# Kernel optimization log

Hardware: AMD Instinct MI355X
Metric: run time of the kernel (lower is better)

The kernel has to match this reference:

```python
import jax, jax.numpy as jnp
import numpy as np

H = 1024
V = 50257
B = 64
T = 512


def setup_inputs() -> dict:
    key = jax.random.key(0)
    ks = jax.random.split(key, 16)
    s = 0.02
    return {
        "input_seq": jax.random.randint(ks[0], (B,), 0, V, dtype=jnp.int32),
        "last_hidden": jax.random.normal(ks[1], (1, B, H), dtype=jnp.float32),
        "encoder_outputs": jax.random.normal(ks[2], (B, T, H), dtype=jnp.float32),
        "emb": jax.random.normal(ks[3], (V, H), dtype=jnp.float32) * s,
        "W_ih": jax.random.normal(ks[4], (3 * H, H), dtype=jnp.float32) * s,
        "W_hh": jax.random.normal(ks[5], (3 * H, H), dtype=jnp.float32) * s,
        "b_ih": jnp.zeros((3 * H,), jnp.float32),
        "b_hh": jnp.zeros((3 * H,), jnp.float32),
        "W_a": jax.random.normal(ks[6], (H, H), dtype=jnp.float32) * s,
        "b_a": jnp.zeros((H,), jnp.float32),
        "W_c": jax.random.normal(ks[7], (H, 2 * H), dtype=jnp.float32) * s,
        "b_c": jnp.zeros((H,), jnp.float32),
        "W_o": jax.random.normal(ks[8], (V, H), dtype=jnp.float32) * s,
        "b_o": jnp.zeros((V,), jnp.float32),
    }


def reference(input_seq, last_hidden, encoder_outputs, emb, W_ih, W_hh, b_ih, b_hh,
              W_a, b_a, W_c, b_c, W_o, b_o):
    # Embedding lookup (dropout is identity in eval)
    x = emb[input_seq]                      # [B, H]
    h0 = last_hidden[0]                     # [B, H] (num_layers == 1)

    # Single GRU step, torch gate order (r, z, n)
    gi = x @ W_ih.T + b_ih                  # [B, 3H]
    gh = h0 @ W_hh.T + b_hh                 # [B, 3H]
    r = jax.nn.sigmoid(gi[:, :H] + gh[:, :H])
    z = jax.nn.sigmoid(gi[:, H:2 * H] + gh[:, H:2 * H])
    n = jnp.tanh(gi[:, 2 * H:] + r * gh[:, 2 * H:])
    h = (1.0 - z) * n + z * h0              # [B, H]

    # Attention, method='general': batched (replaces per-batch torch.mm loop)
    energy = jnp.einsum('bth,oh->bto', encoder_outputs, W_a) + b_a  # [B, T, H]
    scores = jnp.einsum('bh,bth->bt', h, energy)                    # [B, T]
    attn_w = jax.nn.softmax(scores, axis=1)                         # [B, T]
    context = jnp.einsum('bt,bth->bh', attn_w, encoder_outputs)     # [B, H]

    concat_input = jnp.concatenate([h, context], axis=1)            # [B, 2H]
    concat_output = jnp.tanh(concat_input @ W_c.T + b_c)            # [B, H]
    output = concat_output @ W_o.T + b_o                            # [B, V]
    hidden = h[None]                                                # [1, B, H]
    return (output, hidden)
```

## Files before the change

kernel.cpp:

```cpp
#include <hip/hip_runtime.h>
#include <hip/hip_bf16.h>
#include <cstdint>
#include <cstddef>

#define H 1024
#define V 50257
#define B 64
#define T 512

typedef __attribute__((ext_vector_type(8))) short bf16x8;
typedef __attribute__((ext_vector_type(4))) float f32x4;

__device__ __forceinline__ float sigmoidf_(float x) { return 1.0f / (1.0f + expf(-x)); }

__device__ __forceinline__ unsigned short f2bf_rn(float x) {
    __hip_bfloat16 h = __float2bfloat16(x);
    return __builtin_bit_cast(unsigned short, h);
}

__device__ __forceinline__ void gl_lds16(const float* g, float* l) {
    __builtin_amdgcn_global_load_lds(
        (const __attribute__((address_space(1))) unsigned*)g,
        (__attribute__((address_space(3))) unsigned*)l, 16, 0, 0);
}

__device__ __forceinline__ void wave_vm_drain() {
    asm volatile("s_waitcnt vmcnt(0)" ::: "memory");
    __builtin_amdgcn_sched_barrier(0);
}

__global__ void k_prep(const int* __restrict__ seq, const float* __restrict__ emb,
                       const float* __restrict__ h0,
                       unsigned short* __restrict__ X_bf,
                       unsigned short* __restrict__ h0_bf) {
    int i = blockIdx.x * 256 + threadIdx.x;
    int b = i >> 10, h = i & 1023;
    X_bf[i] = f2bf_rn(emb[(size_t)seq[b] * H + h]);
    h0_bf[i] = f2bf_rn(h0[i]);
}

__global__ __launch_bounds__(256) void k_mfma_bt(
    const unsigned short* __restrict__ A0, const unsigned short* __restrict__ A1, int lda,
    const float* __restrict__ B0, const float* __restrict__ B1, int ldb,
    float* __restrict__ C0, float* __restrict__ C1, int N, int KC) {
    __shared__ __align__(16) float Bs[2][128 * 64];
    const unsigned short* A = blockIdx.z ? A1 : A0;
    const float* Bm = blockIdx.z ? B1 : B0;
    float* C = (blockIdx.z ? C1 : C0) + (size_t)blockIdx.y * 64 * N;
    const int t = threadIdx.x;
    const int w = t >> 6, lane = t & 63;
    const int li = lane & 15, qu = lane >> 4;
    const int n0 = blockIdx.x * 128;
    const int k0 = blockIdx.y * KC;
    const int nsteps = KC >> 6;

    f32x4 acc[4][2];
#pragma unroll
    for (int ms = 0; ms < 4; ++ms)
#pragma unroll
        for (int nt = 0; nt < 2; ++nt) acc[ms][nt] = (f32x4){0.f, 0.f, 0.f, 0.f};

#define STG(BUF, KK)                                                            \
    {                                                                           \
        _Pragma("unroll")                                                       \
        for (int j = 0; j < 8; ++j) {                                           \
            int cidx = (w * 8 + j) * 64 + lane;                                 \
            int row = cidx >> 4, cs = cidx & 15;                                \
            int cg = cs ^ (row & 15);                                           \
            const float* gp = Bm + (size_t)(n0 + row) * ldb + (KK) + cg * 4;    \
            gl_lds16(gp, &Bs[BUF][(w * 8 + j) * 256]);                          \
        }                                                                       \
    }

    STG(0, k0)

    for (int kt = 0; kt < nsteps; ++kt) {
        const int buf = kt & 1;
        wave_vm_drain();
        if (kt + 1 < nsteps) STG(buf ^ 1, k0 + (kt + 1) * 64)

        const int kk = k0 + kt * 64;
#pragma unroll
        for (int ks = 0; ks < 2; ++ks) {
            bf16x8 af[4];
#pragma unroll
            for (int ms = 0; ms < 4; ++ms)
                af[ms] = *(const bf16x8*)&A[(size_t)(ms * 16 + li) * lda + kk + ks * 32 + qu * 8];
#pragma unroll
            for (int nt = 0; nt < 2; ++nt) {
                int row = w * 32 + nt * 16 + li;
                int cc0 = ks * 8 + qu * 2;
                float4 x0 = *(const float4*)&Bs[buf][row * 64 + ((cc0)     ^ (row & 15)) * 4];
                float4 x1 = *(const float4*)&Bs[buf][row * 64 + ((cc0 + 1) ^ (row & 15)) * 4];
                bf16x8 bfr;
                bfr[0] = (short)f2bf_rn(x0.x); bfr[1] = (short)f2bf_rn(x0.y);
                bfr[2] = (short)f2bf_rn(x0.z); bfr[3] = (short)f2bf_rn(x0.w);
                bfr[4] = (short)f2bf_rn(x1.x); bfr[5] = (short)f2bf_rn(x1.y);
                bfr[6] = (short)f2bf_rn(x1.z); bfr[7] = (short)f2bf_rn(x1.w);
#pragma unroll
                for (int ms = 0; ms < 4; ++ms)
                    acc[ms][nt] = __builtin_amdgcn_mfma_f32_16x16x32_bf16(
                        af[ms], bfr, acc[ms][nt], 0, 0, 0);
            }
        }
    }
#undef STG

#pragma unroll
    for (int nt = 0; nt < 2; ++nt) {
        int col = n0 + w * 32 + nt * 16 + li;
#pragma unroll
        for (int ms = 0; ms < 4; ++ms)
#pragma unroll
            for (int j = 0; j < 4; ++j)
                C[(size_t)(ms * 16 + qu * 4 + j) * N + col] = acc[ms][nt][j];
    }
}

__global__ __launch_bounds__(256) void k_mfma_wa(const unsigned short* __restrict__ cat_bf,
                                                 const float* __restrict__ Wa,
                                                 float* __restrict__ Pu) {
    const int t = threadIdx.x;
    const int w = t >> 6, lane = t & 63;
    const int li = lane & 15, qu = lane >> 4;
    const int n0 = blockIdx.x * 128;
    const int k0 = blockIdx.y * 256;

    f32x4 acc[4][2];
#pragma unroll
    for (int ms = 0; ms < 4; ++ms)
#pragma unroll
        for (int nt = 0; nt < 2; ++nt) acc[ms][nt] = (f32x4){0.f, 0.f, 0.f, 0.f};

    for (int kt = 0; kt < 4; ++kt) {
        const int kk = k0 + kt * 64;
#pragma unroll
        for (int ks = 0; ks < 2; ++ks) {
            bf16x8 af[4];
#pragma unroll
            for (int ms = 0; ms < 4; ++ms)
                af[ms] = *(const bf16x8*)&cat_bf[(size_t)(ms * 16 + li) * 2048 + kk + ks * 32 + qu * 8];
            const int kb = kk + ks * 32 + qu * 8;
#pragma unroll
            for (int nt = 0; nt < 2; ++nt) {
                int col = n0 + w * 32 + nt * 16 + li;
                bf16x8 bfr;
#pragma unroll
                for (int e = 0; e < 8; ++e)
                    bfr[e] = (short)f2bf_rn(Wa[(size_t)(kb + e) * H + col]);
#pragma unroll
                for (int ms = 0; ms < 4; ++ms)
                    acc[ms][nt] = __builtin_amdgcn_mfma_f32_16x16x32_bf16(
                        af[ms], bfr, acc[ms][nt], 0, 0, 0);
            }
        }
    }
    float* C = Pu + (size_t)blockIdx.y * 64 * H;
#pragma unroll
    for (int nt = 0; nt < 2; ++nt) {
        int col = n0 + w * 32 + nt * 16 + li;
#pragma unroll
        for (int ms = 0; ms < 4; ++ms)
#pragma unroll
            for (int j = 0; j < 4; ++j)
                C[(size_t)(ms * 16 + qu * 4 + j) * H + col] = acc[ms][nt][j];
    }
}

__global__ void k_gru(const float* __restrict__ Pgi, const float* __restrict__ Pgh,
                      const float* __restrict__ bih, const float* __restrict__ bhh,
                      const float* __restrict__ h0, unsigned short* __restrict__ cat_bf,
                      float* __restrict__ hid) {
    int i = blockIdx.x * 256 + threadIdx.x;
    int b = i >> 10, h = i & 1023;
    float gr = bih[h], gz = bih[H + h], gn = bih[2 * H + h];
    float hr = bhh[h], hz = bhh[H + h], hn = bhh[2 * H + h];
#pragma unroll
    for (int kt = 0; kt < 4; ++kt) {
        const float* pi = Pgi + (size_t)kt * B * 3 * H + (size_t)b * 3 * H;
        const float* ph = Pgh + (size_t)kt * B * 3 * H + (size_t)b * 3 * H;
        gr += pi[h]; gz += pi[H + h]; gn += pi[2 * H + h];
        hr += ph[h]; hz += ph[H + h]; hn += ph[2 * H + h];
    }
    float r = sigmoidf_(gr + hr);
    float z = sigmoidf_(gz + hz);
    float n = tanhf(gn + r * hn);
    float hv = (1.0f - z) * n + z * h0[i];
    cat_bf[(size_t)b * 2048 + h] = f2bf_rn(hv);
    hid[i] = hv;
}

__global__ __launch_bounds__(256) void k_flash(const float* __restrict__ Pu,
                                               const float* __restrict__ enc,
                                               float* __restrict__ Pm,
                                               float* __restrict__ Pl,
                                               float* __restrict__ Pc) {
    const int b = blockIdx.x >> 4, ch = blockIdx.x & 15;
    const int w = threadIdx.x >> 6, lane = threadIdx.x & 63;

    float4 uu[4];
#pragma unroll
    for (int it = 0; it < 4; ++it) {
        int col = (it * 64 + lane) * 4;
        float4 s = *(const float4*)&Pu[(size_t)b * H + col];
#pragma unroll
        for (int kt = 1; kt < 4; ++kt) {
            float4 p = *(const float4*)&Pu[(size_t)kt * B * H + (size_t)b * H + col];
            s.x += p.x; s.y += p.y; s.z += p.z; s.w += p.w;
        }
        uu[it] = s;
    }

    float m = -3.4e38f, l = 0.f;
    float4 c[4] = {{0,0,0,0},{0,0,0,0},{0,0,0,0},{0,0,0,0}};
    const float* ebase = enc + ((size_t)b * T + ch * 32 + w * 8) * H;

#pragma unroll 2
    for (int tt = 0; tt < 8; ++tt) {
        float4 e[4];
#pragma unroll
        for (int it = 0; it < 4; ++it)
            e[it] = *(const float4*)&ebase[(size_t)tt * H + (it * 64 + lane) * 4];
        float s = 0.f;
#pragma unroll
        for (int it = 0; it < 4; ++it)
            s += uu[it].x * e[it].x + uu[it].y * e[it].y +
                 uu[it].z * e[it].z + uu[it].w * e[it].w;
#pragma unroll
        for (int o = 32; o; o >>= 1) s += __shfl_xor(s, o, 64);
        float mn = fmaxf(m, s);
        float scale = __expf(m - mn);
        float p = __expf(s - mn);
        l = l * scale + p;
#pragma unroll
        for (int it = 0; it < 4; ++it) {
            c[it].x = fmaf(p, e[it].x, c[it].x * scale);
            c[it].y = fmaf(p, e[it].y, c[it].y * scale);
            c[it].z = fmaf(p, e[it].z, c[it].z * scale);
            c[it].w = fmaf(p, e[it].w, c[it].w * scale);
        }
        m = mn;
    }

    __shared__ float Lm[4], Ll[4];
    __shared__ __align__(16) float Lc[4][H];
#pragma unroll
    for (int it = 0; it < 4; ++it)
        *(float4*)&Lc[w][(it * 64 + lane) * 4] = c[it];
    if (lane == 0) { Lm[w] = m; Ll[w] = l; }
    __syncthreads();

    float M = fmaxf(fmaxf(Lm[0], Lm[1]), fmaxf(Lm[2], Lm[3]));
    float e0 = __expf(Lm[0] - M), e1 = __expf(Lm[1] - M),
          e2 = __expf(Lm[2] - M), e3 = __expf(Lm[3] - M);
    float L = Ll[0] * e0 + Ll[1] * e1 + Ll[2] * e2 + Ll[3] * e3;
    int col = threadIdx.x * 4;
    float4 c0 = *(const float4*)&Lc[0][col];
    float4 c1 = *(const float4*)&Lc[1][col];
    float4 c2 = *(const float4*)&Lc[2][col];
    float4 c3 = *(const float4*)&Lc[3][col];
    float4 cc;
    cc.x = c0.x * e0 + c1.x * e1 + c2.x * e2 + c3.x * e3;
    cc.y = c0.y * e0 + c1.y * e1 + c2.y * e2 + c3.y * e3;
    cc.z = c0.z * e0 + c1.z * e1 + c2.z * e2 + c3.z * e3;
    cc.w = c0.w * e0 + c1.w * e1 + c2.w * e2 + c3.w * e3;
    const int rec = blockIdx.x;
    if (threadIdx.x == 0) { Pm[rec] = M; Pl[rec] = L; }
    *(float4*)&Pc[(size_t)rec * H + col] = cc;
}

__global__ void k_fcomb(const float* __restrict__ Pm, const float* __restrict__ Pl,
                        const float* __restrict__ Pc, unsigned short* __restrict__ cat_bf) {
    const int b = blockIdx.x;
    const int col = threadIdx.x * 4;
    float M = -3.4e38f;
#pragma unroll
    for (int i = 0; i < 16; ++i) M = fmaxf(M, Pm[b * 16 + i]);
    float L = 0.f;
    float4 cc = {0, 0, 0, 0};
#pragma unroll 4
    for (int i = 0; i < 16; ++i) {
        float wgt = __expf(Pm[b * 16 + i] - M);
        L += Pl[b * 16 + i] * wgt;
        float4 p = *(const float4*)&Pc[(size_t)(b * 16 + i) * H + col];
        cc.x += wgt * p.x; cc.y += wgt * p.y;
        cc.z += wgt * p.z; cc.w += wgt * p.w;
    }
    float inv = 1.0f / L;
    ushort4 o;
    o.x = f2bf_rn(cc.x * inv); o.y = f2bf_rn(cc.y * inv);
    o.z = f2bf_rn(cc.z * inv); o.w = f2bf_rn(cc.w * inv);
    *(ushort4*)&cat_bf[(size_t)b * 2048 + 1024 + col] = o;
}

__global__ void k_co(const float* __restrict__ Pc, const float* __restrict__ bc,
                     unsigned short* __restrict__ co_bf) {
    int i = blockIdx.x * 256 + threadIdx.x;
    int h = i & 1023;
    float s = bc[h];
#pragma unroll
    for (int kt = 0; kt < 4; ++kt) s += Pc[kt * (B * H) + i];
    co_bf[i] = f2bf_rn(tanhf(s));
}

__global__ __launch_bounds__(256) void k_out_mfma(const unsigned short* __restrict__ co_bf,
                                                  const float* __restrict__ Wo,
                                                  const float* __restrict__ bo,
                                                  float* __restrict__ out) {
    __shared__ __align__(16) float Bs[2][128 * 64];
    const int t = threadIdx.x;
    const int w = t >> 6, lane = t & 63;
    const int li = lane & 15, qu = lane >> 4;
    const int v0 = blockIdx.x * 128;

    f32x4 acc[4][2];
#pragma unroll
    for (int ms = 0; ms < 4; ++ms)
#pragma unroll
        for (int nt = 0; nt < 2; ++nt) acc[ms][nt] = (f32x4){0.f, 0.f, 0.f, 0.f};

#define STAGE(BUF, KK)                                                          \
    {                                                                           \
        _Pragma("unroll")                                                       \
        for (int j = 0; j < 8; ++j) {                                           \
            int cidx = (w * 8 + j) * 64 + lane;                                 \
            int row = cidx >> 4, cs = cidx & 15;                                \
            int cg = cs ^ (row & 15);                                           \
            int vr = v0 + row; if (vr >= V) vr = V - 1;                         \
            const float* gp = Wo + (size_t)vr * H + (KK) + cg * 4;              \
            gl_lds16(gp, &Bs[BUF][(w * 8 + j) * 256]);                          \
        }                                                                       \
    }

    STAGE(0, 0)

    for (int kt = 0; kt < 16; ++kt) {
        const int buf = kt & 1;
        wave_vm_drain();
        if (kt < 15) STAGE(buf ^ 1, (kt + 1) * 64)

        const int kk = kt * 64;
#pragma unroll
        for (int ks = 0; ks < 2; ++ks) {
            bf16x8 af[4];
#pragma unroll
            for (int ms = 0; ms < 4; ++ms)
                af[ms] = *(const bf16x8*)&co_bf[(size_t)(ms * 16 + li) * H + kk + ks * 32 + qu * 8];
#pragma unroll
            for (int nt = 0; nt < 2; ++nt) {
                int row = w * 32 + nt * 16 + li;
                int cc0 = ks * 8 + qu * 2;
                float4 x0 = *(const float4*)&Bs[buf][row * 64 + ((cc0)     ^ (row & 15)) * 4];
                float4 x1 = *(const float4*)&Bs[buf][row * 64 + ((cc0 + 1) ^ (row & 15)) * 4];
                bf16x8 bfr;
                bfr[0] = (short)f2bf_rn(x0.x); bfr[1] = (short)f2bf_rn(x0.y);
                bfr[2] = (short)f2bf_rn(x0.z); bfr[3] = (short)f2bf_rn(x0.w);
                bfr[4] = (short)f2bf_rn(x1.x); bfr[5] = (short)f2bf_rn(x1.y);
                bfr[6] = (short)f2bf_rn(x1.z); bfr[7] = (short)f2bf_rn(x1.w);
#pragma unroll
                for (int ms = 0; ms < 4; ++ms)
                    acc[ms][nt] = __builtin_amdgcn_mfma_f32_16x16x32_bf16(
                        af[ms], bfr, acc[ms][nt], 0, 0, 0);
            }
        }
    }
#undef STAGE

#pragma unroll
    for (int nt = 0; nt < 2; ++nt) {
        int v = v0 + w * 32 + nt * 16 + li;
        if (v < V) {
            float bov = bo[v];
#pragma unroll
            for (int ms = 0; ms < 4; ++ms)
#pragma unroll
                for (int j = 0; j < 4; ++j)
                    out[(size_t)(ms * 16 + qu * 4 + j) * V + v] = acc[ms][nt][j] + bov;
        }
    }
}

extern "C" void kernel_launch(void* const* d_in, const int* in_sizes, int n_in,
                              void* d_out, int out_size, void* d_ws, size_t ws_size,
                              hipStream_t stream) {
    (void)in_sizes; (void)n_in; (void)out_size; (void)ws_size;
    const int*   seq = (const int*)d_in[0];
    const float* h0  = (const float*)d_in[1];
    const float* enc = (const float*)d_in[2];
    const float* emb = (const float*)d_in[3];
    const float* Wih = (const float*)d_in[4];
    const float* Whh = (const float*)d_in[5];
    const float* bih = (const float*)d_in[6];
    const float* bhh = (const float*)d_in[7];
    const float* Wa  = (const float*)d_in[8];
    const float* Wc  = (const float*)d_in[10];
    const float* bc  = (const float*)d_in[11];
    const float* Wo  = (const float*)d_in[12];
    const float* bo  = (const float*)d_in[13];

    float* out = (float*)d_out;
    float* hid = out + (size_t)B * V;

    float* ws   = (float*)d_ws;
    float* Pgi  = ws;
    float* Pgh  = Pgi + 786432;
    float* Pu   = Pgh + 786432;
    float* Pm   = Pu + 262144;
    float* Pl   = Pm + 1024;
    float* Pc   = Pl + 1024;
    float* Pcg  = Pc + 1048576;
    unsigned short* X_bf  = (unsigned short*)(Pcg + 262144);
    unsigned short* h0_bf = X_bf + 65536;
    unsigned short* cat_bf = h0_bf + 65536;
    unsigned short* co_bf  = cat_bf + 131072;

    k_prep<<<256, 256, 0, stream>>>(seq, emb, h0, X_bf, h0_bf);
    k_mfma_bt<<<dim3(24, 4, 2), 256, 0, stream>>>(X_bf, h0_bf, H, Wih, Whh, H,
                                                  Pgi, Pgh, 3 * H, 256);
    k_gru<<<256, 256, 0, stream>>>(Pgi, Pgh, bih, bhh, h0, cat_bf, hid);
    k_mfma_wa<<<dim3(8, 4), 256, 0, stream>>>(cat_bf, Wa, Pu);
    k_flash<<<1024, 256, 0, stream>>>(Pu, enc, Pm, Pl, Pc);
    k_fcomb<<<64, 256, 0, stream>>>(Pm, Pl, Pc, cat_bf);
    k_mfma_bt<<<dim3(8, 4, 1), 256, 0, stream>>>(cat_bf, cat_bf, 2 * H, Wc, Wc, 2 * H,
                                                 Pcg, Pcg, H, 512);
    k_co<<<256, 256, 0, stream>>>(Pcg, bc, co_bf);
    k_out_mfma<<<(V + 127) / 128, 256, 0, stream>>>(co_bf, Wo, bo, out);
}
```

Before: 142.4 us.

## Deepen GEMM prefetch pipeline and fuse embedding prep into gates GEMM

```diff
diff --git a/kernel.cpp b/kernel.cpp
--- a/kernel.cpp
+++ b/kernel.cpp
@@ -24,29 +24,125 @@
         (__attribute__((address_space(3))) unsigned*)l, 16, 0, 0);
 }
 
-__device__ __forceinline__ void wave_vm_drain() {
+__device__ __forceinline__ void wait_vm8() {
+    asm volatile("s_waitcnt vmcnt(8)" ::: "memory");
+    __builtin_amdgcn_sched_barrier(0);
+}
+__device__ __forceinline__ void wait_vm0() {
     asm volatile("s_waitcnt vmcnt(0)" ::: "memory");
     __builtin_amdgcn_sched_barrier(0);
 }
-
-__global__ void k_prep(const int* __restrict__ seq, const float* __restrict__ emb,
-                       const float* __restrict__ h0,
-                       unsigned short* __restrict__ X_bf,
-                       unsigned short* __restrict__ h0_bf) {
-    int i = blockIdx.x * 256 + threadIdx.x;
-    int b = i >> 10, h = i & 1023;
-    X_bf[i] = f2bf_rn(emb[(size_t)seq[b] * H + h]);
-    h0_bf[i] = f2bf_rn(h0[i]);
-}
-
-__global__ __launch_bounds__(256) void k_mfma_bt(
-    const unsigned short* __restrict__ A0, const unsigned short* __restrict__ A1, int lda,
-    const float* __restrict__ B0, const float* __restrict__ B1, int ldb,
-    float* __restrict__ C0, float* __restrict__ C1, int N, int KC) {
+__device__ __forceinline__ void lds_war_guard() {
+    asm volatile("s_waitcnt lgkmcnt(0)" ::: "memory");
+    __builtin_amdgcn_sched_barrier(0);
+}
+
+__global__ __launch_bounds__(256) void k_gates(const int* __restrict__ seq,
+                                               const float* __restrict__ emb,
+                                               const float* __restrict__ h0,
+                                               const float* __restrict__ Wih,
+                                               const float* __restrict__ Whh,
+                                               float* __restrict__ Pgi,
+                                               float* __restrict__ Pgh) {
     __shared__ __align__(16) float Bs[2][128 * 64];
-    const unsigned short* A = blockIdx.z ? A1 : A0;
-    const float* Bm = blockIdx.z ? B1 : B0;
-    float* C = (blockIdx.z ? C1 : C0) + (size_t)blockIdx.y * 64 * N;
+    const int z = blockIdx.z;
+    const float* Bm = z ? Whh : Wih;
+    float* C = (z ? Pgh : Pgi) + (size_t)blockIdx.y * 64 * (3 * H);
+    const int t = threadIdx.x;
+    const int w = t >> 6, lane = t & 63;
+    const int li = lane & 15, qu = lane >> 4;
+    const int n0 = blockIdx.x * 128;
+    const int k0 = blockIdx.y * 256;
+    const int N = 3 * H;
+
+    const float* Arow[4];
+#pragma unroll
+    for (int ms = 0; ms < 4; ++ms) {
+        int m = ms * 16 + li;
+        Arow[ms] = z ? (h0 + (size_t)m * H) : (emb + (size_t)seq[m] * H);
+    }
+
+    f32x4 acc[4][2];
+#pragma unroll
+    for (int ms = 0; ms < 4; ++ms)
+#pragma unroll
+        for (int nt = 0; nt < 2; ++nt) acc[ms][nt] = (f32x4){0.f, 0.f, 0.f, 0.f};
+
+#define STG(BUF, KK)                                                            \
+    {                                                                           \
+        _Pragma("unroll")                                                       \
+        for (int j = 0; j < 8; ++j) {                                           \
+            int cidx = (w * 8 + j) * 64 + lane;                                 \
+            int row = cidx >> 4, cs = cidx & 15;                                \
+            int cg = cs ^ (row & 15);                                           \
+            const float* gp = Bm + (size_t)(n0 + row) * H + (KK) + cg * 4;      \
+            gl_lds16(gp, &Bs[BUF][(w * 8 + j) * 256]);                          \
+        }                                                                       \
+    }
+
+#define CONSUME(BUF, KK)                                                        \
+    {                                                                           \
+        _Pragma("unroll")                                                       \
+        for (int ks = 0; ks < 2; ++ks) {                                        \
+            bf16x8 af[4];                                                       \
+            _Pragma("unroll")                                                   \
+            for (int ms = 0; ms < 4; ++ms) {                                    \
+                float4 a0 = *(const float4*)&Arow[ms][(KK) + ks * 32 + qu * 8]; \
+                float4 a1 = *(const float4*)&Arow[ms][(KK) + ks * 32 + qu * 8 + 4]; \
+                af[ms][0] = (short)f2bf_rn(a0.x); af[ms][1] = (short)f2bf_rn(a0.y); \
+                af[ms][2] = (short)f2bf_rn(a0.z); af[ms][3] = (short)f2bf_rn(a0.w); \
+                af[ms][4] = (short)f2bf_rn(a1.x); af[ms][5] = (short)f2bf_rn(a1.y); \
+                af[ms][6] = (short)f2bf_rn(a1.z); af[ms][7] = (short)f2bf_rn(a1.w); \
+            }                                                                   \
+            _Pragma("unroll")                                                   \
+            for (int nt = 0; nt < 2; ++nt) {                                    \
+                int row = w * 32 + nt * 16 + li;                                \
+                int cc0 = ks * 8 + qu * 2;                                      \
+                float4 x0 = *(const float4*)&Bs[BUF][row * 64 + ((cc0)     ^ (row & 15)) * 4]; \
+                float4 x1 = *(const float4*)&Bs[BUF][row * 64 + ((cc0 + 1) ^ (row & 15)) * 4]; \
+                bf16x8 bfr;                                                     \
+                bfr[0] = (short)f2bf_rn(x0.x); bfr[1] = (short)f2bf_rn(x0.y);   \
+                bfr[2] = (short)f2bf_rn(x0.z); bfr[3] = (short)f2bf_rn(x0.w);   \
+                bfr[4] = (short)f2bf_rn(x1.x); bfr[5] = (short)f2bf_rn(x1.y);   \
+                bfr[6] = (short)f2bf_rn(x1.z); bfr[7] = (short)f2bf_rn(x1.w);   \
+                _Pragma("unroll")                                               \
+                for (int ms = 0; ms < 4; ++ms)                                  \
+                    acc[ms][nt] = __builtin_amdgcn_mfma_f32_16x16x32_bf16(      \
+                        af[ms], bfr, acc[ms][nt], 0, 0, 0);                     \
+            }                                                                   \
+        }                                                                       \
+    }
+
+    STG(0, k0)
+    STG(1, k0 + 64)
+    for (int kt = 0; kt < 3; ++kt) {
+        const int buf = kt & 1;
+        wait_vm8();
+        CONSUME(buf, k0 + kt * 64)
+        if (kt + 2 < 4) { lds_war_guard(); STG(buf, k0 + (kt + 2) * 64) }
+    }
+    wait_vm0();
+    CONSUME(1, k0 + 3 * 64)
+#undef STG
+#undef CONSUME
+
+#pragma unroll
+    for (int nt = 0; nt < 2; ++nt) {
+        int col = n0 + w * 32 + nt * 16 + li;
+#pragma unroll
+        for (int ms = 0; ms < 4; ++ms)
+#pragma unroll
+            for (int j = 0; j < 4; ++j)
+                C[(size_t)(ms * 16 + qu * 4 + j) * N + col] = acc[ms][nt][j];
+    }
+}
+
+__global__ __launch_bounds__(256) void k_mfma_bt(const unsigned short* __restrict__ A,
+                                                 int lda,
+                                                 const float* __restrict__ Bm, int ldb,
+                                                 float* __restrict__ Cp, int N, int KC) {
+    __shared__ __align__(16) float Bs[2][128 * 64];
+    float* C = Cp + (size_t)blockIdx.y * 64 * N;
     const int t = threadIdx.x;
     const int w = t >> 6, lane = t & 63;
     const int li = lane & 15, qu = lane >> 4;
@@ -72,39 +168,45 @@
         }                                                                       \
     }
 
+#define CONSUME(BUF, KK)                                                        \
+    {                                                                           \
+        _Pragma("unroll")                                                       \
+        for (int ks = 0; ks < 2; ++ks) {                                        \
+            bf16x8 af[4];                                                       \
+            _Pragma("unroll")                                                   \
+            for (int ms = 0; ms < 4; ++ms)                                      \
+                af[ms] = *(const bf16x8*)&A[(size_t)(ms * 16 + li) * lda + (KK) + ks * 32 + qu * 8]; \
+            _Pragma("unroll")                                                   \
+            for (int nt = 0; nt < 2; ++nt) {                                    \
+                int row = w * 32 + nt * 16 + li;                                \
+                int cc0 = ks * 8 + qu * 2;                                      \
+                float4 x0 = *(const float4*)&Bs[BUF][row * 64 + ((cc0)     ^ (row & 15)) * 4]; \
+                float4 x1 = *(const float4*)&Bs[BUF][row * 64 + ((cc0 + 1) ^ (row & 15)) * 4]; \
+                bf16x8 bfr;                                                     \
+                bfr[0] = (short)f2bf_rn(x0.x); bfr[1] = (short)f2bf_rn(x0.y);   \
+                bfr[2] = (short)f2bf_rn(x0.z); bfr[3] = (short)f2bf_rn(x0.w);   \
+                bfr[4] = (short)f2bf_rn(x1.x); bfr[5] = (short)f2bf_rn(x1.y);   \
+                bfr[6] = (short)f2bf_rn(x1.z); bfr[7] = (short)f2bf_rn(x1.w);   \
+                _Pragma("unroll")                                               \
+                for (int ms = 0; ms < 4; ++ms)                                  \
+                    acc[ms][nt] = __builtin_amdgcn_mfma_f32_16x16x32_bf16(      \
+                        af[ms], bfr, acc[ms][nt], 0, 0, 0);                     \
+            }                                                                   \
+        }                                                                       \
+    }
+
     STG(0, k0)
-
-    for (int kt = 0; kt < nsteps; ++kt) {
+    STG(1, k0 + 64)
+    for (int kt = 0; kt < nsteps - 1; ++kt) {
         const int buf = kt & 1;
-        wave_vm_drain();
-        if (kt + 1 < nsteps) STG(buf ^ 1, k0 + (kt + 1) * 64)
-
-        const int kk = k0 + kt * 64;
-#pragma unroll
-        for (int ks = 0; ks < 2; ++ks) {
-            bf16x8 af[4];
-#pragma unroll
-            for (int ms = 0; ms < 4; ++ms)
-                af[ms] = *(const bf16x8*)&A[(size_t)(ms * 16 + li) * lda + kk + ks * 32 + qu * 8];
-#pragma unroll
-            for (int nt = 0; nt < 2; ++nt) {
-                int row = w * 32 + nt * 16 + li;
-                int cc0 = ks * 8 + qu * 2;
-                float4 x0 = *(const float4*)&Bs[buf][row * 64 + ((cc0)     ^ (row & 15)) * 4];
-                float4 x1 = *(const float4*)&Bs[buf][row * 64 + ((cc0 + 1) ^ (row & 15)) * 4];
-                bf16x8 bfr;
-                bfr[0] = (short)f2bf_rn(x0.x); bfr[1] = (short)f2bf_rn(x0.y);
-                bfr[2] = (short)f2bf_rn(x0.z); bfr[3] = (short)f2bf_rn(x0.w);
-                bfr[4] = (short)f2bf_rn(x1.x); bfr[5] = (short)f2bf_rn(x1.y);
-                bfr[6] = (short)f2bf_rn(x1.z); bfr[7] = (short)f2bf_rn(x1.w);
-#pragma unroll
-                for (int ms = 0; ms < 4; ++ms)
-                    acc[ms][nt] = __builtin_amdgcn_mfma_f32_16x16x32_bf16(
-                        af[ms], bfr, acc[ms][nt], 0, 0, 0);
-            }
-        }
-    }
+        wait_vm8();
+        CONSUME(buf, k0 + kt * 64)
+        if (kt + 2 < nsteps) { lds_war_guard(); STG(buf, k0 + (kt + 2) * 64) }
+    }
+    wait_vm0();
+    CONSUME((nsteps - 1) & 1, k0 + (nsteps - 1) * 64)
 #undef STG
+#undef CONSUME
 
 #pragma unroll
     for (int nt = 0; nt < 2; ++nt) {
@@ -332,39 +434,45 @@
         }                                                                       \
     }
 
+#define CONSUME(BUF, KK)                                                        \
+    {                                                                           \
+        _Pragma("unroll")                                                       \
+        for (int ks = 0; ks < 2; ++ks) {                                        \
+            bf16x8 af[4];                                                       \
+            _Pragma("unroll")                                                   \
+            for (int ms = 0; ms < 4; ++ms)                                      \
+                af[ms] = *(const bf16x8*)&co_bf[(size_t)(ms * 16 + li) * H + (KK) + ks * 32 + qu * 8]; \
+            _Pragma("unroll")                                                   \
+            for (int nt = 0; nt < 2; ++nt) {                                    \
+                int row = w * 32 + nt * 16 + li;                                \
+                int cc0 = ks * 8 + qu * 2;                                      \
+                float4 x0 = *(const float4*)&Bs[BUF][row * 64 + ((cc0)     ^ (row & 15)) * 4]; \
+                float4 x1 = *(const float4*)&Bs[BUF][row * 64 + ((cc0 + 1) ^ (row & 15)) * 4]; \
+                bf16x8 bfr;                                                     \
+                bfr[0] = (short)f2bf_rn(x0.x); bfr[1] = (short)f2bf_rn(x0.y);   \
+                bfr[2] = (short)f2bf_rn(x0.z); bfr[3] = (short)f2bf_rn(x0.w);   \
+                bfr[4] = (short)f2bf_rn(x1.x); bfr[5] = (short)f2bf_rn(x1.y);   \
+                bfr[6] = (short)f2bf_rn(x1.z); bfr[7] = (short)f2bf_rn(x1.w);   \
+                _Pragma("unroll")                                               \
+                for (int ms = 0; ms < 4; ++ms)                                  \
+                    acc[ms][nt] = __builtin_amdgcn_mfma_f32_16x16x32_bf16(      \
+                        af[ms], bfr, acc[ms][nt], 0, 0, 0);                     \
+            }                                                                   \
+        }                                                                       \
+    }
+
     STAGE(0, 0)
-
-    for (int kt = 0; kt < 16; ++kt) {
+    STAGE(1, 64)
+    for (int kt = 0; kt < 15; ++kt) {
         const int buf = kt & 1;
-        wave_vm_drain();
-        if (kt < 15) STAGE(buf ^ 1, (kt + 1) * 64)
-
-        const int kk = kt * 64;
-#pragma unroll
-        for (int ks = 0; ks < 2; ++ks) {
-            bf16x8 af[4];
-#pragma unroll
-            for (int ms = 0; ms < 4; ++ms)
-                af[ms] = *(const bf16x8*)&co_bf[(size_t)(ms * 16 + li) * H + kk + ks * 32 + qu * 8];
-#pragma unroll
-            for (int nt = 0; nt < 2; ++nt) {
-                int row = w * 32 + nt * 16 + li;
-                int cc0 = ks * 8 + qu * 2;
-                float4 x0 = *(const float4*)&Bs[buf][row * 64 + ((cc0)     ^ (row & 15)) * 4];
-                float4 x1 = *(const float4*)&Bs[buf][row * 64 + ((cc0 + 1) ^ (row & 15)) * 4];
-                bf16x8 bfr;
-                bfr[0] = (short)f2bf_rn(x0.x); bfr[1] = (short)f2bf_rn(x0.y);
-                bfr[2] = (short)f2bf_rn(x0.z); bfr[3] = (short)f2bf_rn(x0.w);
-                bfr[4] = (short)f2bf_rn(x1.x); bfr[5] = (short)f2bf_rn(x1.y);
-                bfr[6] = (short)f2bf_rn(x1.z); bfr[7] = (short)f2bf_rn(x1.w);
-#pragma unroll
-                for (int ms = 0; ms < 4; ++ms)
-                    acc[ms][nt] = __builtin_amdgcn_mfma_f32_16x16x32_bf16(
-                        af[ms], bfr, acc[ms][nt], 0, 0, 0);
-            }
-        }
-    }
+        wait_vm8();
+        CONSUME(buf, kt * 64)
+        if (kt + 2 < 16) { lds_war_guard(); STAGE(buf, (kt + 2) * 64) }
+    }
+    wait_vm0();
+    CONSUME(1, 15 * 64)
 #undef STAGE
+#undef CONSUME
 
 #pragma unroll
     for (int nt = 0; nt < 2; ++nt) {
@@ -409,20 +517,15 @@
     float* Pl   = Pm + 1024;
     float* Pc   = Pl + 1024;
     float* Pcg  = Pc + 1048576;
-    unsigned short* X_bf  = (unsigned short*)(Pcg + 262144);
-    unsigned short* h0_bf = X_bf + 65536;
-    unsigned short* cat_bf = h0_bf + 65536;
+    unsigned short* cat_bf = (unsigned short*)(Pcg + 262144);
     unsigned short* co_bf  = cat_bf + 131072;
 
-    k_prep<<<256, 256, 0, stream>>>(seq, emb, h0, X_bf, h0_bf);
-    k_mfma_bt<<<dim3(24, 4, 2), 256, 0, stream>>>(X_bf, h0_bf, H, Wih, Whh, H,
-                                                  Pgi, Pgh, 3 * H, 256);
+    k_gates<<<dim3(24, 4, 2), 256, 0, stream>>>(seq, emb, h0, Wih, Whh, Pgi, Pgh);
     k_gru<<<256, 256, 0, stream>>>(Pgi, Pgh, bih, bhh, h0, cat_bf, hid);
     k_mfma_wa<<<dim3(8, 4), 256, 0, stream>>>(cat_bf, Wa, Pu);
     k_flash<<<1024, 256, 0, stream>>>(Pu, enc, Pm, Pl, Pc);
     k_fcomb<<<64, 256, 0, stream>>>(Pm, Pl, Pc, cat_bf);
-    k_mfma_bt<<<dim3(8, 4, 1), 256, 0, stream>>>(cat_bf, cat_bf, 2 * H, Wc, Wc, 2 * H,
-                                                 Pcg, Pcg, H, 512);
+    k_mfma_bt<<<dim3(8, 4), 256, 0, stream>>>(cat_bf, 2 * H, Wc, 2 * H, Pcg, H, 512);
     k_co<<<256, 256, 0, stream>>>(Pcg, bc, co_bf);
     k_out_mfma<<<(V + 127) / 128, 256, 0, stream>>>(co_bf, Wo, bo, out);
 }
```

Result: no change. 142.4 us (-0.0%).
